# Kernel optimization log

Measured on AMD Instinct MI355X. Metric: run time of the kernel, lower is better.

## Reference

```python
import jax, jax.numpy as jnp
import numpy as np
from jax import lax

# ---- Loihi neuron constants (params['neuron'], params['simulation']) ----
VTH_MANT = 80
THETA = VTH_MANT * (1 << 6)          # 5120, vThMant scaled by 2^6 weight resolution
I_DECAY = 1024                        # current decay (12-bit fixed point)
V_DECAY = 128                         # voltage decay (12-bit fixed point)
WGT_EXP = 0
WGT_SCALE = 1 << (6 + WGT_EXP)        # 64
TS = 1.0

def _loihi_srm_kernel():
    # integer Loihi simulation of the PSP impulse response (slayerLoihi._calculateLoihiPSP)
    u = 1 << (6 + WGT_EXP)
    v = u
    ker = [v]
    while ker[-1] > 0:
        u = (u * (4096 - I_DECAY)) >> 12
        v = ((v * (4096 - V_DECAY)) >> 12) + u
        ker.append(v)
    return np.asarray(ker, np.float32) / (1 << 6)

SRM_KERNEL = _loihi_srm_kernel()      # ~180 taps, ker[0] = 1

def psp(x):
    # causal FIR over time: y[t] = sum_k x[t-k] * ker[k];  x: [B, C, T]
    B, C, T = x.shape
    K = SRM_KERNEL.shape[0]
    w = jnp.asarray(SRM_KERNEL[::-1].copy()).reshape(1, 1, K).astype(x.dtype)
    y = lax.conv_general_dilated(x.reshape(B * C, 1, T), w, (1,), [(K - 1, 0)],
                                 dimension_numbers=('NCH', 'OIH', 'NCH'))
    return y.reshape(B, C, T)

def _decay(x, d):
    # sign-symmetric arithmetic-shift decay, exactly as the Loihi CUDA kernel
    s = jnp.where(x >= 0, 1, -1).astype(jnp.int32)
    return s * ((s * x * (4096 - d)) >> 12)

def spike_loihi(w):
    # quantized integrate-and-fire; w: [B, C, T] float weighted input
    x = jnp.trunc(w * (WGT_SCALE / TS)).astype(jnp.int32)   # C-style int() truncation
    xt = jnp.moveaxis(x, -1, 0)                             # [T, B, C]
    z = jnp.zeros(x.shape[:-1], jnp.int32)
    def step(carry, xi):
        u, v = carry
        un = _decay(u, I_DECAY) + xi
        vn = _decay(v, V_DECAY) + un
        sp = vn >= THETA
        vn = jnp.where(sp, 0, vn)                           # hard reset on spike
        return (un, vn), (sp, vn)
    _, (s, vrec) = lax.scan(step, (z, z), xt)
    spike = jnp.moveaxis(s, 0, -1).astype(w.dtype) / TS
    voltage = jnp.moveaxis(vrec, 0, -1).astype(w.dtype)
    return spike, voltage

def delay_shift(x):
    # delayShift(x, 1): one-tick axonal delay along time
    return jnp.concatenate([jnp.zeros_like(x[..., :1]), x[..., :-1]], axis=-1)

def setup_inputs():
    key = jax.random.key(0)
    k1, k2, k3 = jax.random.split(key, 3)
    B, CIN, HID, COUT, T = 32, 512, 1024, 256, 512
    spike_input = (jax.random.uniform(k1, (B, CIN, 1, 1, T)) < 0.05).astype(jnp.float32)
    W1 = jax.random.normal(k2, (HID, CIN), jnp.float32) * 0.2
    W2 = jax.random.normal(k3, (COUT, HID), jnp.float32) * 0.2
    return {"spike_input": spike_input, "W1": W1, "W2": W2}

def reference(spike_input, W1, W2):
    x = spike_input[:, :, 0, 0, :]                          # [B, Cin, T]
    s1, _ = spike_loihi(psp(jnp.einsum('oi,bit->bot', W1, x)))
    s1 = delay_shift(s1)
    s2, _ = spike_loihi(psp(jnp.einsum('oh,bht->bot', W2, s1)))
    s2 = delay_shift(s2)
    return s2[:, :, None, None, :]                          # [B, Cout, 1, 1, T]
```

## Files before the change

kernel.cpp:

```cpp
#include <hip/hip_runtime.h>


#pragma clang fp contract(off)

constexpr int kT     = 512;
constexpr int kCIN   = 512;
constexpr int kHID   = 1024;
constexpr int kCOUT  = 256;
constexpr int kB     = 32;
constexpr int kTHETA = 5120;
constexpr int kOT1   = 16;
constexpr int kOT2   = 8;
constexpr int kHP1   = 20;
constexpr int kHP2   = 12;
constexpr int kSBP   = 516;
constexpr int kCURP  = 522;
constexpr int kLCAP  = 128;

struct Ker { float v[96]; int n; };
constexpr Ker mk_ker() {
    Ker K{}; int u = 64, v = 64; K.v[0] = 1.0f; int i = 1;
    while (v > 0 && i < 96) {
        u = (u * 3072) >> 12;
        v = ((v * 3968) >> 12) + u;
        K.v[i++] = (float)v / 64.0f;
    }
    K.n = i; return K;
}
constexpr Ker KER = mk_ker();
static_assert(KER.n == 88, "SRM kernel length must be 88");
static_assert(KER.v[87] == 0.0f, "tap 87 must be the exact zero tail tap");
__device__ __constant__ Ker KERC = mk_ker();

__device__ __forceinline__ float2 pkmul(const float2 a, const float b) {
    return make_float2(a.x * b, a.y * b);
}
__device__ __forceinline__ float2 pkadd(const float2 a, const float2 b) {
    return make_float2(a.x + b.x, a.y + b.y);
}

__device__ __forceinline__ int decay_i(int x, int mult) {
    unsigned ax = (x >= 0) ? (unsigned)x : (0u - (unsigned)x);
    unsigned p  = ax * (unsigned)mult;
    int sh = ((int)p) >> 12;
    return (x >= 0) ? sh : (int)(0u - (unsigned)sh);
}

__global__ __launch_bounds__(256) void k0_pack(const float* __restrict__ X,
                                               unsigned* __restrict__ XPW) {
    const int tid = blockIdx.x * 256 + threadIdx.x;
    const int b = tid >> 13, rem = tid & 8191, w = rem >> 9, t = rem & 511;
    const float* xp = X + ((size_t)(b * kCIN + w * 32)) * kT + t;
    unsigned m = 0;
#pragma unroll
    for (int k = 0; k < 32; ++k)
        m |= (xp[(size_t)k * kT] != 0.0f ? 1u : 0u) << k;
    XPW[tid] = m;
}

__global__ __launch_bounds__(256) void k0b_list(const unsigned* __restrict__ XPW,
                                                unsigned short* __restrict__ XL,
                                                unsigned short* __restrict__ XC) {
    const int bt = blockIdx.x * 256 + threadIdx.x;
    const int b = bt >> 9, t = bt & 511;
    const unsigned* xw = XPW + ((size_t)b * 16) * kT + t;
    unsigned short* row = XL + (size_t)bt * kLCAP;
    int cnt = 0;
    for (int w = 0; w < 16; ++w) {
        unsigned m = xw[(size_t)w * kT];
        while (m) {
            const int bi = __ffs(m) - 1; m &= m - 1;
            if (cnt < kLCAP) row[cnt] = (unsigned short)(w * 32 + bi);
            ++cnt;
        }
    }
    XC[bt] = (unsigned short)min(cnt, kLCAP);
}

#define GADD16(II) { const int ii_ = (II); \
    const float4 f0 = *reinterpret_cast<const float4*>(&w0[ii_ * 4]); \
    const float4 f1 = *reinterpret_cast<const float4*>(&w1[ii_ * 4]); \
    const float4 f2 = *reinterpret_cast<const float4*>(&w2[ii_ * 4]); \
    const float4 f3 = *reinterpret_cast<const float4*>(&w3[ii_ * 4]); \
    A0 = pkadd(A0, make_float2(f0.x, f0.y)); A1 = pkadd(A1, make_float2(f0.z, f0.w)); \
    A2 = pkadd(A2, make_float2(f1.x, f1.y)); A3 = pkadd(A3, make_float2(f1.z, f1.w)); \
    A4 = pkadd(A4, make_float2(f2.x, f2.y)); A5 = pkadd(A5, make_float2(f2.z, f2.w)); \
    A6 = pkadd(A6, make_float2(f3.x, f3.y)); A7 = pkadd(A7, make_float2(f3.z, f3.w)); }

#define ACC16(E0,E1,E2,E3,E4,E5,E6,E7, Q0,Q1,Q2,Q3, KV) \
    E0 = pkadd(E0, pkmul(make_float2(Q0.x, Q0.y), (KV))); \
    E1 = pkadd(E1, pkmul(make_float2(Q0.z, Q0.w), (KV))); \
    E2 = pkadd(E2, pkmul(make_float2(Q1.x, Q1.y), (KV))); \
    E3 = pkadd(E3, pkmul(make_float2(Q1.z, Q1.w), (KV))); \
    E4 = pkadd(E4, pkmul(make_float2(Q2.x, Q2.y), (KV))); \
    E5 = pkadd(E5, pkmul(make_float2(Q2.z, Q2.w), (KV))); \
    E6 = pkadd(E6, pkmul(make_float2(Q3.x, Q3.y), (KV))); \
    E7 = pkadd(E7, pkmul(make_float2(Q3.z, Q3.w), (KV)));

__global__ __launch_bounds__(512, 6) void k1_fused(const unsigned short* __restrict__ XL,
                                                   const unsigned short* __restrict__ XC,
                                                   const float* __restrict__ W,
                                                   unsigned short* __restrict__ SPW) {
    __shared__ __align__(16) unsigned char regn[40960];
    __shared__ unsigned char sbuf[kOT1 * kSBP];

    float* w0    = reinterpret_cast<float*>(regn);
    float* w1    = reinterpret_cast<float*>(regn + 8192);
    float* w2    = reinterpret_cast<float*>(regn + 16384);
    float* w3    = reinterpret_cast<float*>(regn + 24576);
    float* heven = reinterpret_cast<float*>(regn);
    float* hodd  = reinterpret_cast<float*>(regn + 20480);
    int*   cur   = reinterpret_cast<int*>(regn);

    const int t     = threadIdx.x;
    const int b     = blockIdx.x >> 6;
    const int oblk  = blockIdx.x & 63;
    const int obase = oblk * kOT1;

    for (int idx = t; idx < kOT1 * kCIN; idx += 512) {
        const int j = idx >> 9, i = idx & 511;
        float* wq = reinterpret_cast<float*>(regn + (j >> 2) * 8192);
        wq[i * 4 + (j & 3)] = W[(size_t)(obase + j) * kCIN + i];
    }
    __syncthreads();

    const int bt = (b << 9) | t;
    const int cnt = XC[bt];
    const uint4* lrow = reinterpret_cast<const uint4*>(XL + (size_t)bt * kLCAP);
    float2 A0 = make_float2(0.f, 0.f), A1 = A0, A2 = A0, A3 = A0,
           A4 = A0, A5 = A0, A6 = A0, A7 = A0;
    for (int k8 = 0; k8 * 8 < cnt; ++k8) {
        const uint4 le = lrow[k8];
        const int base = k8 * 8;
#define GE1(E, V) if (base + (E) < cnt) GADD16((int)(V))
        GE1(0, le.x & 0xffffu) GE1(1, le.x >> 16)
        GE1(2, le.y & 0xffffu) GE1(3, le.y >> 16)
        GE1(4, le.z & 0xffffu) GE1(5, le.z >> 16)
        GE1(6, le.w & 0xffffu) GE1(7, le.w >> 16)
#undef GE1
    }
    __syncthreads();

    {
        float* hr = ((t & 1) ? hodd : heven) + (size_t)(t >> 1) * kHP1;
        *reinterpret_cast<float4*>(hr + 0)  = make_float4(A0.x, A0.y, A1.x, A1.y);
        *reinterpret_cast<float4*>(hr + 4)  = make_float4(A2.x, A2.y, A3.x, A3.y);
        *reinterpret_cast<float4*>(hr + 8)  = make_float4(A4.x, A4.y, A5.x, A5.y);
        *reinterpret_cast<float4*>(hr + 12) = make_float4(A6.x, A6.y, A7.x, A7.y);
    }
    __syncthreads();

    float2 E0, E1, E2, E3, E4, E5, E6, E7, O0, O1, O2, O3, O4, O5, O6, O7;
    E0=E1=E2=E3=E4=E5=E6=E7=O0=O1=O2=O3=O4=O5=O6=O7 = make_float2(0.f, 0.f);
    const int q = t;
    if (t < 256) {
        for (int j = 0; j < 43; ++j) {
            const int m = q - 43 + j;
            const float t87 = KERC.v[87 - 2 * j];
            const float t86 = KERC.v[86 - 2 * j];
            const float t85 = KERC.v[85 - 2 * j];
            if (m >= 0) {
                const float* he = heven + (size_t)m * kHP1;
                const float* ho = hodd  + (size_t)m * kHP1;
                const float4 a0 = *reinterpret_cast<const float4*>(he + 0);
                const float4 a1 = *reinterpret_cast<const float4*>(he + 4);
                const float4 a2 = *reinterpret_cast<const float4*>(he + 8);
                const float4 a3 = *reinterpret_cast<const float4*>(he + 12);
                const float4 b0 = *reinterpret_cast<const float4*>(ho + 0);
                const float4 b1 = *reinterpret_cast<const float4*>(ho + 4);
                const float4 b2 = *reinterpret_cast<const float4*>(ho + 8);
                const float4 b3 = *reinterpret_cast<const float4*>(ho + 12);
                ACC16(E0,E1,E2,E3,E4,E5,E6,E7, a0,a1,a2,a3, t86)
                ACC16(E0,E1,E2,E3,E4,E5,E6,E7, b0,b1,b2,b3, t85)
                ACC16(O0,O1,O2,O3,O4,O5,O6,O7, a0,a1,a2,a3, t87)
                ACC16(O0,O1,O2,O3,O4,O5,O6,O7, b0,b1,b2,b3, t86)
            }
        }
        {
            const float* he = heven + (size_t)q * kHP1;
            const float* ho = hodd  + (size_t)q * kHP1;
            const float4 a0 = *reinterpret_cast<const float4*>(he + 0);
            const float4 a1 = *reinterpret_cast<const float4*>(he + 4);
            const float4 a2 = *reinterpret_cast<const float4*>(he + 8);
            const float4 a3 = *reinterpret_cast<const float4*>(he + 12);
            const float4 b0 = *reinterpret_cast<const float4*>(ho + 0);
            const float4 b1 = *reinterpret_cast<const float4*>(ho + 4);
            const float4 b2 = *reinterpret_cast<const float4*>(ho + 8);
            const float4 b3 = *reinterpret_cast<const float4*>(ho + 12);
            const float v1 = KERC.v[1];
            ACC16(E0,E1,E2,E3,E4,E5,E6,E7, a0,a1,a2,a3, 1.0f)
            ACC16(O0,O1,O2,O3,O4,O5,O6,O7, a0,a1,a2,a3, v1)
            ACC16(O0,O1,O2,O3,O4,O5,O6,O7, b0,b1,b2,b3, 1.0f)
        }
    }
    __syncthreads();

    if (t < 256) {
#define CST1(CH, EV, OV) \
        *reinterpret_cast<int2*>(cur + (CH) * kCURP + 2 * q) = \
            make_int2((int)((EV) * 64.0f), (int)((OV) * 64.0f));
        CST1( 0, E0.x, O0.x) CST1( 1, E0.y, O0.y)
        CST1( 2, E1.x, O1.x) CST1( 3, E1.y, O1.y)
        CST1( 4, E2.x, O2.x) CST1( 5, E2.y, O2.y)
        CST1( 6, E3.x, O3.x) CST1( 7, E3.y, O3.y)
        CST1( 8, E4.x, O4.x) CST1( 9, E4.y, O4.y)
        CST1(10, E5.x, O5.x) CST1(11, E5.y, O5.y)
        CST1(12, E6.x, O6.x) CST1(13, E6.y, O6.y)
        CST1(14, E7.x, O7.x) CST1(15, E7.y, O7.y)
#undef CST1
    }
    __syncthreads();

    if (t < kOT1) {
        const int2* cr2 = reinterpret_cast<const int2*>(cur + t * kCURP);
        int u = 0, v = 0;
        sbuf[t * kSBP + 0] = 0;
        for (int s2 = 0; s2 < 256; ++s2) {
            const int2 c2 = cr2[s2];
            {
                const int un = (int)((unsigned)decay_i(u, 3072) + (unsigned)c2.x);
                int vn = (int)((unsigned)decay_i(v, 3968) + (unsigned)un);
                const int sp_ = (vn >= kTHETA) ? 1 : 0;
                if (sp_) vn = 0;
                u = un; v = vn;
                sbuf[t * kSBP + 2 * s2 + 1] = (unsigned char)sp_;
            }
            {
                const int un = (int)((unsigned)decay_i(u, 3072) + (unsigned)c2.y);
                int vn = (int)((unsigned)decay_i(v, 3968) + (unsigned)un);
                const int sp_ = (vn >= kTHETA) ? 1 : 0;
                if (sp_) vn = 0;
                u = un; v = vn;
                if (2 * s2 + 2 < kT) sbuf[t * kSBP + 2 * s2 + 2] = (unsigned char)sp_;
            }
        }
    }
    __syncthreads();

    {
        unsigned lo = 0, hi = 0;
#pragma unroll
        for (int j = 0; j < 8; ++j) {
            lo |= (unsigned)sbuf[j * kSBP + t] << j;
            hi |= (unsigned)sbuf[(8 + j) * kSBP + t] << j;
        }
        SPW[((((size_t)b * 32 + (oblk >> 1)) * kT) + t) * 2 + (oblk & 1)] =
            (unsigned short)(lo | (hi << 8));
    }
}

#define GW8(MW, BASE) { unsigned m_ = (MW); while (m_) { \
    const int bi_ = __ffs(m_) - 1; m_ &= m_ - 1; const int ii_ = (BASE) + bi_; \
    const float4 lo = *reinterpret_cast<const float4*>(&wlo[ii_ * 4]); \
    const float4 hi = *reinterpret_cast<const float4*>(&whi[ii_ * 4]); \
    A0 = pkadd(A0, make_float2(lo.x, lo.y)); A1 = pkadd(A1, make_float2(lo.z, lo.w)); \
    A2 = pkadd(A2, make_float2(hi.x, hi.y)); A3 = pkadd(A3, make_float2(hi.z, hi.w)); } }

#define ACC8(E0,E1,E2,E3, Q0,Q1, KV) \
    E0 = pkadd(E0, pkmul(make_float2(Q0.x, Q0.y), (KV))); \
    E1 = pkadd(E1, pkmul(make_float2(Q0.z, Q0.w), (KV))); \
    E2 = pkadd(E2, pkmul(make_float2(Q1.x, Q1.y), (KV))); \
    E3 = pkadd(E3, pkmul(make_float2(Q1.z, Q1.w), (KV)));

__global__ __launch_bounds__(512, 8) void k2_fused(const unsigned* __restrict__ SPW,
                                                   const float* __restrict__ W,
                                                   float* __restrict__ O) {
    __shared__ __align__(16) unsigned char regn[32768];
    __shared__ unsigned char sbuf[kOT2 * kSBP];

    float* wlo   = reinterpret_cast<float*>(regn);
    float* whi   = reinterpret_cast<float*>(regn + 16384);
    float* heven = reinterpret_cast<float*>(regn);
    float* hodd  = reinterpret_cast<float*>(regn + 12288);
    int*   cur   = reinterpret_cast<int*>(regn);

    const int t     = threadIdx.x;
    const int b     = blockIdx.x >> 5;
    const int obase = (blockIdx.x & 31) * kOT2;

    for (int idx = t; idx < kOT2 * kHID; idx += 512) {
        const int j = idx >> 10, i = idx & 1023;
        const float w = W[(size_t)(obase + j) * kHID + i];
        if (j < 4) wlo[i * 4 + j] = w; else whi[i * 4 + (j - 4)] = w;
    }
    __syncthreads();

    const unsigned* sp = SPW + ((size_t)b * 32) * kT + t;
    float2 A0 = make_float2(0.f, 0.f), A1 = A0, A2 = A0, A3 = A0;
#pragma unroll 4
    for (int g = 0; g < 32; ++g) {
        const unsigned m = sp[(size_t)g * kT];
        GW8(m, g * 32)
    }
    __syncthreads();

    {
        float* hr = ((t & 1) ? hodd : heven) + (size_t)(t >> 1) * kHP2;
        *reinterpret_cast<float4*>(hr + 0) = make_float4(A0.x, A0.y, A1.x, A1.y);
        *reinterpret_cast<float4*>(hr + 4) = make_float4(A2.x, A2.y, A3.x, A3.y);
    }
    __syncthreads();

    float2 E0, E1, E2, E3, O0, O1, O2, O3;
    E0=E1=E2=E3=O0=O1=O2=O3 = make_float2(0.f, 0.f);
    const int q = t;
    if (t < 256) {
        for (int j = 0; j < 43; ++j) {
            const int m = q - 43 + j;
            const float t87 = KERC.v[87 - 2 * j];
            const float t86 = KERC.v[86 - 2 * j];
            const float t85 = KERC.v[85 - 2 * j];
            if (m >= 0) {
                const float* he = heven + (size_t)m * kHP2;
                const float* ho = hodd  + (size_t)m * kHP2;
                const float4 a0 = *reinterpret_cast<const float4*>(he + 0);
                const float4 a1 = *reinterpret_cast<const float4*>(he + 4);
                const float4 b0 = *reinterpret_cast<const float4*>(ho + 0);
                const float4 b1 = *reinterpret_cast<const float4*>(ho + 4);
                ACC8(E0,E1,E2,E3, a0,a1, t86)
                ACC8(E0,E1,E2,E3, b0,b1, t85)
                ACC8(O0,O1,O2,O3, a0,a1, t87)
                ACC8(O0,O1,O2,O3, b0,b1, t86)
            }
        }
        {
            const float* he = heven + (size_t)q * kHP2;
            const float* ho = hodd  + (size_t)q * kHP2;
            const float4 a0 = *reinterpret_cast<const float4*>(he + 0);
            const float4 a1 = *reinterpret_cast<const float4*>(he + 4);
            const float4 b0 = *reinterpret_cast<const float4*>(ho + 0);
            const float4 b1 = *reinterpret_cast<const float4*>(ho + 4);
            const float v1 = KERC.v[1];
            ACC8(E0,E1,E2,E3, a0,a1, 1.0f)
            ACC8(O0,O1,O2,O3, a0,a1, v1)
            ACC8(O0,O1,O2,O3, b0,b1, 1.0f)
        }
    }
    __syncthreads();

    if (t < 256) {
#define CST2(CH, EV, OV) \
        *reinterpret_cast<int2*>(cur + (CH) * kCURP + 2 * q) = \
            make_int2((int)((EV) * 64.0f), (int)((OV) * 64.0f));
        CST2(0, E0.x, O0.x) CST2(1, E0.y, O0.y)
        CST2(2, E1.x, O1.x) CST2(3, E1.y, O1.y)
        CST2(4, E2.x, O2.x) CST2(5, E2.y, O2.y)
        CST2(6, E3.x, O3.x) CST2(7, E3.y, O3.y)
#undef CST2
    }
    __syncthreads();

    if (t < kOT2) {
        const int2* cr2 = reinterpret_cast<const int2*>(cur + t * kCURP);
        int u = 0, v = 0;
        sbuf[t * kSBP + 0] = 0;
        for (int s2 = 0; s2 < 256; ++s2) {
            const int2 c2 = cr2[s2];
            {
                const int un = (int)((unsigned)decay_i(u, 3072) + (unsigned)c2.x);
                int vn = (int)((unsigned)decay_i(v, 3968) + (unsigned)un);
                const int sp2 = (vn >= kTHETA) ? 1 : 0;
                if (sp2) vn = 0;
                u = un; v = vn;
                sbuf[t * kSBP + 2 * s2 + 1] = (unsigned char)sp2;
            }
            {
                const int un = (int)((unsigned)decay_i(u, 3072) + (unsigned)c2.y);
                int vn = (int)((unsigned)decay_i(v, 3968) + (unsigned)un);
                const int sp2 = (vn >= kTHETA) ? 1 : 0;
                if (sp2) vn = 0;
                u = un; v = vn;
                if (2 * s2 + 2 < kT) sbuf[t * kSBP + 2 * s2 + 2] = (unsigned char)sp2;
            }
        }
    }
    __syncthreads();

    for (int idx = t; idx < kOT2 * kT; idx += 512) {
        const int j = idx >> 9, tt = idx & 511;
        O[((size_t)(b * kCOUT + obase + j)) * kT + tt] = (float)sbuf[j * kSBP + tt];
    }
}

__global__ void k_mark(float* __restrict__ out0, float v) {
    if (threadIdx.x == 0 && blockIdx.x == 0) out0[0] = v;
}

extern "C" void kernel_launch(void* const* d_in, const int* in_sizes, int n_in,
                              void* d_out, int out_size, void* d_ws, size_t ws_size,
                              hipStream_t stream) {
    const float* X  = (const float*)d_in[0];
    const float* W1 = (const float*)d_in[1];
    const float* W2 = (const float*)d_in[2];
    float* OUT = (float*)d_out;

    const size_t xpw_bytes = (size_t)kB * 16 * kT * 4;
    const size_t spw_bytes = (size_t)kB * 32 * kT * 4;
    const size_t xl_bytes  = (size_t)kB * kT * kLCAP * 2;
    const size_t xc_bytes  = (size_t)kB * kT * 2;
    const size_t need = xpw_bytes + spw_bytes + xl_bytes + xc_bytes;

    if (n_in != 3 || in_sizes[0] != kB * kCIN * kT || in_sizes[1] != kHID * kCIN ||
        in_sizes[2] != kCOUT * kHID || out_size != kB * kCOUT * kT) {
        hipLaunchKernelGGL(k_mark, dim3(1), dim3(64), 0, stream, OUT, 7000001.0f);
        return;
    }
    if (ws_size < need || d_ws == nullptr) {
        const float v = (float)(8000000u + (unsigned)((ws_size >> 10) % 900000));
        hipLaunchKernelGGL(k_mark, dim3(1), dim3(64), 0, stream, OUT, v);
        return;
    }

    char* ws = (char*)d_ws;
    unsigned*       xpw = (unsigned*)ws;
    unsigned short* spw = (unsigned short*)(ws + xpw_bytes);
    unsigned short* xl  = (unsigned short*)(ws + xpw_bytes + spw_bytes);
    unsigned short* xc  = (unsigned short*)(ws + xpw_bytes + spw_bytes + xl_bytes);

    hipLaunchKernelGGL(k0_pack, dim3(kB * 16 * kT / 256), dim3(256), 0, stream,
                       X, xpw);
    hipLaunchKernelGGL(k0b_list, dim3(kB * kT / 256), dim3(256), 0, stream,
                       xpw, xl, xc);
    hipLaunchKernelGGL(k1_fused, dim3(kB * (kHID / kOT1)), dim3(512), 0, stream,
                       xl, xc, W1, spw);
    hipLaunchKernelGGL(k2_fused, dim3(kB * (kCOUT / kOT2)), dim3(512), 0, stream,
                       (const unsigned*)spw, W2, OUT);
}
```

Baseline: 390.5 us.

## Move part of weight tiles from LDS to pre-packed global reads; split PSP across all threads

Result: slower. 442.6 us (+13.3%).

```diff
diff --git a/kernel.cpp b/kernel.cpp
--- a/kernel.cpp
+++ b/kernel.cpp
@@ -77,29 +77,40 @@
     XC[bt] = (unsigned short)min(cnt, kLCAP);
 }
 
+__global__ __launch_bounds__(256) void k0c_w1p(const float* __restrict__ W1,
+                                               float* __restrict__ W1P) {
+    const int tid = blockIdx.x * 256 + threadIdx.x;
+    const int c = tid & 3, i = (tid >> 2) & 511, oblk = tid >> 11;
+    W1P[tid] = W1[(size_t)(oblk * 16 + 12 + c) * kCIN + i];
+}
+
+__global__ __launch_bounds__(256) void k0d_w2p(const float* __restrict__ W2,
+                                               float* __restrict__ W2P) {
+    const int tid = blockIdx.x * 256 + threadIdx.x;
+    const int c = tid & 3, i = (tid >> 2) & 1023, o2 = tid >> 12;
+    W2P[tid] = W2[(size_t)(o2 * 8 + 4 + c) * kHID + i];
+}
+
 #define GADD16(II) { const int ii_ = (II); \
     const float4 f0 = *reinterpret_cast<const float4*>(&w0[ii_ * 4]); \
     const float4 f1 = *reinterpret_cast<const float4*>(&w1[ii_ * 4]); \
     const float4 f2 = *reinterpret_cast<const float4*>(&w2[ii_ * 4]); \
-    const float4 f3 = *reinterpret_cast<const float4*>(&w3[ii_ * 4]); \
+    const float4 f3 = w1p4[ii_];   \
     A0 = pkadd(A0, make_float2(f0.x, f0.y)); A1 = pkadd(A1, make_float2(f0.z, f0.w)); \
     A2 = pkadd(A2, make_float2(f1.x, f1.y)); A3 = pkadd(A3, make_float2(f1.z, f1.w)); \
     A4 = pkadd(A4, make_float2(f2.x, f2.y)); A5 = pkadd(A5, make_float2(f2.z, f2.w)); \
     A6 = pkadd(A6, make_float2(f3.x, f3.y)); A7 = pkadd(A7, make_float2(f3.z, f3.w)); }
 
-#define ACC16(E0,E1,E2,E3,E4,E5,E6,E7, Q0,Q1,Q2,Q3, KV) \
+#define ACC8(E0,E1,E2,E3, Q0,Q1, KV) \
     E0 = pkadd(E0, pkmul(make_float2(Q0.x, Q0.y), (KV))); \
     E1 = pkadd(E1, pkmul(make_float2(Q0.z, Q0.w), (KV))); \
     E2 = pkadd(E2, pkmul(make_float2(Q1.x, Q1.y), (KV))); \
-    E3 = pkadd(E3, pkmul(make_float2(Q1.z, Q1.w), (KV))); \
-    E4 = pkadd(E4, pkmul(make_float2(Q2.x, Q2.y), (KV))); \
-    E5 = pkadd(E5, pkmul(make_float2(Q2.z, Q2.w), (KV))); \
-    E6 = pkadd(E6, pkmul(make_float2(Q3.x, Q3.y), (KV))); \
-    E7 = pkadd(E7, pkmul(make_float2(Q3.z, Q3.w), (KV)));
+    E3 = pkadd(E3, pkmul(make_float2(Q1.z, Q1.w), (KV)));
 
 __global__ __launch_bounds__(512, 6) void k1_fused(const unsigned short* __restrict__ XL,
                                                    const unsigned short* __restrict__ XC,
                                                    const float* __restrict__ W,
+                                                   const float* __restrict__ W1P,
                                                    unsigned short* __restrict__ SPW) {
     __shared__ __align__(16) unsigned char regn[40960];
     __shared__ unsigned char sbuf[kOT1 * kSBP];
@@ -107,7 +118,6 @@
     float* w0    = reinterpret_cast<float*>(regn);
     float* w1    = reinterpret_cast<float*>(regn + 8192);
     float* w2    = reinterpret_cast<float*>(regn + 16384);
-    float* w3    = reinterpret_cast<float*>(regn + 24576);
     float* heven = reinterpret_cast<float*>(regn);
     float* hodd  = reinterpret_cast<float*>(regn + 20480);
     int*   cur   = reinterpret_cast<int*>(regn);
@@ -117,7 +127,9 @@
     const int oblk  = blockIdx.x & 63;
     const int obase = oblk * kOT1;
 
-    for (int idx = t; idx < kOT1 * kCIN; idx += 512) {
+    const float4* w1p4 = reinterpret_cast<const float4*>(W1P + (size_t)oblk * kCIN * 4);
+
+    for (int idx = t; idx < 12 * kCIN; idx += 512) {
         const int j = idx >> 9, i = idx & 511;
         float* wq = reinterpret_cast<float*>(regn + (j >> 2) * 8192);
         wq[i * 4 + (j & 3)] = W[(size_t)(obase + j) * kCIN + i];
@@ -150,63 +162,49 @@
     }
     __syncthreads();
 
-    float2 E0, E1, E2, E3, E4, E5, E6, E7, O0, O1, O2, O3, O4, O5, O6, O7;
-    E0=E1=E2=E3=E4=E5=E6=E7=O0=O1=O2=O3=O4=O5=O6=O7 = make_float2(0.f, 0.f);
-    const int q = t;
-    if (t < 256) {
-        for (int j = 0; j < 43; ++j) {
-            const int m = q - 43 + j;
-            const float t87 = KERC.v[87 - 2 * j];
-            const float t86 = KERC.v[86 - 2 * j];
-            const float t85 = KERC.v[85 - 2 * j];
-            if (m >= 0) {
-                const float* he = heven + (size_t)m * kHP1;
-                const float* ho = hodd  + (size_t)m * kHP1;
-                const float4 a0 = *reinterpret_cast<const float4*>(he + 0);
-                const float4 a1 = *reinterpret_cast<const float4*>(he + 4);
-                const float4 a2 = *reinterpret_cast<const float4*>(he + 8);
-                const float4 a3 = *reinterpret_cast<const float4*>(he + 12);
-                const float4 b0 = *reinterpret_cast<const float4*>(ho + 0);
-                const float4 b1 = *reinterpret_cast<const float4*>(ho + 4);
-                const float4 b2 = *reinterpret_cast<const float4*>(ho + 8);
-                const float4 b3 = *reinterpret_cast<const float4*>(ho + 12);
-                ACC16(E0,E1,E2,E3,E4,E5,E6,E7, a0,a1,a2,a3, t86)
-                ACC16(E0,E1,E2,E3,E4,E5,E6,E7, b0,b1,b2,b3, t85)
-                ACC16(O0,O1,O2,O3,O4,O5,O6,O7, a0,a1,a2,a3, t87)
-                ACC16(O0,O1,O2,O3,O4,O5,O6,O7, b0,b1,b2,b3, t86)
-            }
-        }
-        {
-            const float* he = heven + (size_t)q * kHP1;
-            const float* ho = hodd  + (size_t)q * kHP1;
+    const int p = t & 255, half = t >> 8, hoff = half * 8;
+    float2 E0, E1, E2, E3, O0, O1, O2, O3;
+    E0=E1=E2=E3=O0=O1=O2=O3 = make_float2(0.f, 0.f);
+    for (int j = 0; j < 43; ++j) {
+        const int m = p - 43 + j;
+        const float t87 = KERC.v[87 - 2 * j];
+        const float t86 = KERC.v[86 - 2 * j];
+        const float t85 = KERC.v[85 - 2 * j];
+        if (m >= 0) {
+            const float* he = heven + (size_t)m * kHP1 + hoff;
+            const float* ho = hodd  + (size_t)m * kHP1 + hoff;
             const float4 a0 = *reinterpret_cast<const float4*>(he + 0);
             const float4 a1 = *reinterpret_cast<const float4*>(he + 4);
-            const float4 a2 = *reinterpret_cast<const float4*>(he + 8);
-            const float4 a3 = *reinterpret_cast<const float4*>(he + 12);
             const float4 b0 = *reinterpret_cast<const float4*>(ho + 0);
             const float4 b1 = *reinterpret_cast<const float4*>(ho + 4);
-            const float4 b2 = *reinterpret_cast<const float4*>(ho + 8);
-            const float4 b3 = *reinterpret_cast<const float4*>(ho + 12);
-            const float v1 = KERC.v[1];
-            ACC16(E0,E1,E2,E3,E4,E5,E6,E7, a0,a1,a2,a3, 1.0f)
-            ACC16(O0,O1,O2,O3,O4,O5,O6,O7, a0,a1,a2,a3, v1)
-            ACC16(O0,O1,O2,O3,O4,O5,O6,O7, b0,b1,b2,b3, 1.0f)
-        }
-    }
-    __syncthreads();
-
-    if (t < 256) {
+            ACC8(E0,E1,E2,E3, a0,a1, t86)
+            ACC8(E0,E1,E2,E3, b0,b1, t85)
+            ACC8(O0,O1,O2,O3, a0,a1, t87)
+            ACC8(O0,O1,O2,O3, b0,b1, t86)
+        }
+    }
+    {
+        const float* he = heven + (size_t)p * kHP1 + hoff;
+        const float* ho = hodd  + (size_t)p * kHP1 + hoff;
+        const float4 a0 = *reinterpret_cast<const float4*>(he + 0);
+        const float4 a1 = *reinterpret_cast<const float4*>(he + 4);
+        const float4 b0 = *reinterpret_cast<const float4*>(ho + 0);
+        const float4 b1 = *reinterpret_cast<const float4*>(ho + 4);
+        const float v1 = KERC.v[1];
+        ACC8(E0,E1,E2,E3, a0,a1, 1.0f)
+        ACC8(O0,O1,O2,O3, a0,a1, v1)
+        ACC8(O0,O1,O2,O3, b0,b1, 1.0f)
+    }
+    __syncthreads();
+
+    {
 #define CST1(CH, EV, OV) \
-        *reinterpret_cast<int2*>(cur + (CH) * kCURP + 2 * q) = \
+        *reinterpret_cast<int2*>(cur + (CH) * kCURP + 2 * p) = \
             make_int2((int)((EV) * 64.0f), (int)((OV) * 64.0f));
-        CST1( 0, E0.x, O0.x) CST1( 1, E0.y, O0.y)
-        CST1( 2, E1.x, O1.x) CST1( 3, E1.y, O1.y)
-        CST1( 4, E2.x, O2.x) CST1( 5, E2.y, O2.y)
-        CST1( 6, E3.x, O3.x) CST1( 7, E3.y, O3.y)
-        CST1( 8, E4.x, O4.x) CST1( 9, E4.y, O4.y)
-        CST1(10, E5.x, O5.x) CST1(11, E5.y, O5.y)
-        CST1(12, E6.x, O6.x) CST1(13, E6.y, O6.y)
-        CST1(14, E7.x, O7.x) CST1(15, E7.y, O7.y)
+        CST1(hoff + 0, E0.x, O0.x) CST1(hoff + 1, E0.y, O0.y)
+        CST1(hoff + 2, E1.x, O1.x) CST1(hoff + 3, E1.y, O1.y)
+        CST1(hoff + 4, E2.x, O2.x) CST1(hoff + 5, E2.y, O2.y)
+        CST1(hoff + 6, E3.x, O3.x) CST1(hoff + 7, E3.y, O3.y)
 #undef CST1
     }
     __syncthreads();
@@ -252,36 +250,32 @@
 #define GW8(MW, BASE) { unsigned m_ = (MW); while (m_) { \
     const int bi_ = __ffs(m_) - 1; m_ &= m_ - 1; const int ii_ = (BASE) + bi_; \
     const float4 lo = *reinterpret_cast<const float4*>(&wlo[ii_ * 4]); \
-    const float4 hi = *reinterpret_cast<const float4*>(&whi[ii_ * 4]); \
+    const float4 hi = w2p4[ii_];   \
     A0 = pkadd(A0, make_float2(lo.x, lo.y)); A1 = pkadd(A1, make_float2(lo.z, lo.w)); \
     A2 = pkadd(A2, make_float2(hi.x, hi.y)); A3 = pkadd(A3, make_float2(hi.z, hi.w)); } }
 
-#define ACC8(E0,E1,E2,E3, Q0,Q1, KV) \
-    E0 = pkadd(E0, pkmul(make_float2(Q0.x, Q0.y), (KV))); \
-    E1 = pkadd(E1, pkmul(make_float2(Q0.z, Q0.w), (KV))); \
-    E2 = pkadd(E2, pkmul(make_float2(Q1.x, Q1.y), (KV))); \
-    E3 = pkadd(E3, pkmul(make_float2(Q1.z, Q1.w), (KV)));
-
 __global__ __launch_bounds__(512, 8) void k2_fused(const unsigned* __restrict__ SPW,
                                                    const float* __restrict__ W,
+                                                   const float* __restrict__ W2P,
                                                    float* __restrict__ O) {
-    __shared__ __align__(16) unsigned char regn[32768];
+    __shared__ __align__(16) unsigned char regn[24576];
     __shared__ unsigned char sbuf[kOT2 * kSBP];
 
     float* wlo   = reinterpret_cast<float*>(regn);
-    float* whi   = reinterpret_cast<float*>(regn + 16384);
     float* heven = reinterpret_cast<float*>(regn);
     float* hodd  = reinterpret_cast<float*>(regn + 12288);
     int*   cur   = reinterpret_cast<int*>(regn);
 
     const int t     = threadIdx.x;
     const int b     = blockIdx.x >> 5;
-    const int obase = (blockIdx.x & 31) * kOT2;
-
-    for (int idx = t; idx < kOT2 * kHID; idx += 512) {
+    const int o2    = blockIdx.x & 31;
+    const int obase = o2 * kOT2;
+
+    const float4* w2p4 = reinterpret_cast<const float4*>(W2P + (size_t)o2 * kHID * 4);
+
+    for (int idx = t; idx < 4 * kHID; idx += 512) {
         const int j = idx >> 10, i = idx & 1023;
-        const float w = W[(size_t)(obase + j) * kHID + i];
-        if (j < 4) wlo[i * 4 + j] = w; else whi[i * 4 + (j - 4)] = w;
+        wlo[i * 4 + j] = W[(size_t)(obase + j) * kHID + i];
     }
     __syncthreads();
 
@@ -398,7 +392,10 @@
     const size_t spw_bytes = (size_t)kB * 32 * kT * 4;
     const size_t xl_bytes  = (size_t)kB * kT * kLCAP * 2;
     const size_t xc_bytes  = (size_t)kB * kT * 2;
-    const size_t need = xpw_bytes + spw_bytes + xl_bytes + xc_bytes;
+    const size_t w1p_bytes = (size_t)64 * kCIN * 4 * 4;
+    const size_t w2p_bytes = (size_t)32 * kHID * 4 * 4;
+    const size_t need = xpw_bytes + spw_bytes + xl_bytes + xc_bytes +
+                        w1p_bytes + w2p_bytes;
 
     if (n_in != 3 || in_sizes[0] != kB * kCIN * kT || in_sizes[1] != kHID * kCIN ||
         in_sizes[2] != kCOUT * kHID || out_size != kB * kCOUT * kT) {
@@ -416,13 +413,19 @@
     unsigned short* spw = (unsigned short*)(ws + xpw_bytes);
     unsigned short* xl  = (unsigned short*)(ws + xpw_bytes + spw_bytes);
     unsigned short* xc  = (unsigned short*)(ws + xpw_bytes + spw_bytes + xl_bytes);
+    float*          w1p = (float*)(ws + xpw_bytes + spw_bytes + xl_bytes + xc_bytes);
+    float*          w2p = (float*)(ws + xpw_bytes + spw_bytes + xl_bytes + xc_bytes + w1p_bytes);
 
     hipLaunchKernelGGL(k0_pack, dim3(kB * 16 * kT / 256), dim3(256), 0, stream,
                        X, xpw);
     hipLaunchKernelGGL(k0b_list, dim3(kB * kT / 256), dim3(256), 0, stream,
                        xpw, xl, xc);
+    hipLaunchKernelGGL(k0c_w1p, dim3(64 * kCIN * 4 / 256), dim3(256), 0, stream,
+                       W1, w1p);
+    hipLaunchKernelGGL(k0d_w2p, dim3(32 * kHID * 4 / 256), dim3(256), 0, stream,
+                       W2, w2p);
     hipLaunchKernelGGL(k1_fused, dim3(kB * (kHID / kOT1)), dim3(512), 0, stream,
-                       xl, xc, W1, spw);
+                       xl, xc, W1, w1p, spw);
     hipLaunchKernelGGL(k2_fused, dim3(kB * (kCOUT / kOT2)), dim3(512), 0, stream,
-                       (const unsigned*)spw, W2, OUT);
-}
+                       (const unsigned*)spw, W2, w2p, OUT);
+}
```

## Use all 512 threads for layer-1 PSP with 4-phase polyphase split

Applied to the files above, without the earlier changes.

New measurement: 381.0 us (median of 3 runs). 1.02x faster.

```diff
diff --git a/kernel.cpp b/kernel.cpp
--- a/kernel.cpp
+++ b/kernel.cpp
@@ -14,7 +14,8 @@
 constexpr int kHP1   = 20;
 constexpr int kHP2   = 12;
 constexpr int kSBP   = 516;
-constexpr int kCURP  = 522;
+constexpr int kCURP1 = 524;
+constexpr int kCURP2 = 522;
 constexpr int kLCAP  = 128;
 
 struct Ker { float v[96]; int n; };
@@ -87,15 +88,9 @@
     A4 = pkadd(A4, make_float2(f2.x, f2.y)); A5 = pkadd(A5, make_float2(f2.z, f2.w)); \
     A6 = pkadd(A6, make_float2(f3.x, f3.y)); A7 = pkadd(A7, make_float2(f3.z, f3.w)); }
 
-#define ACC16(E0,E1,E2,E3,E4,E5,E6,E7, Q0,Q1,Q2,Q3, KV) \
-    E0 = pkadd(E0, pkmul(make_float2(Q0.x, Q0.y), (KV))); \
-    E1 = pkadd(E1, pkmul(make_float2(Q0.z, Q0.w), (KV))); \
-    E2 = pkadd(E2, pkmul(make_float2(Q1.x, Q1.y), (KV))); \
-    E3 = pkadd(E3, pkmul(make_float2(Q1.z, Q1.w), (KV))); \
-    E4 = pkadd(E4, pkmul(make_float2(Q2.x, Q2.y), (KV))); \
-    E5 = pkadd(E5, pkmul(make_float2(Q2.z, Q2.w), (KV))); \
-    E6 = pkadd(E6, pkmul(make_float2(Q3.x, Q3.y), (KV))); \
-    E7 = pkadd(E7, pkmul(make_float2(Q3.z, Q3.w), (KV)));
+#define ACCROW(CA, CB, R, KV) \
+    CA = pkadd(CA, pkmul(make_float2((R).x, (R).y), (KV))); \
+    CB = pkadd(CB, pkmul(make_float2((R).z, (R).w), (KV)));
 
 __global__ __launch_bounds__(512, 6) void k1_fused(const unsigned short* __restrict__ XL,
                                                    const unsigned short* __restrict__ XC,
@@ -104,13 +99,11 @@
     __shared__ __align__(16) unsigned char regn[40960];
     __shared__ unsigned char sbuf[kOT1 * kSBP];
 
-    float* w0    = reinterpret_cast<float*>(regn);
-    float* w1    = reinterpret_cast<float*>(regn + 8192);
-    float* w2    = reinterpret_cast<float*>(regn + 16384);
-    float* w3    = reinterpret_cast<float*>(regn + 24576);
-    float* heven = reinterpret_cast<float*>(regn);
-    float* hodd  = reinterpret_cast<float*>(regn + 20480);
-    int*   cur   = reinterpret_cast<int*>(regn);
+    float* w0 = reinterpret_cast<float*>(regn);
+    float* w1 = reinterpret_cast<float*>(regn + 8192);
+    float* w2 = reinterpret_cast<float*>(regn + 16384);
+    float* w3 = reinterpret_cast<float*>(regn + 24576);
+    int*   cur = reinterpret_cast<int*>(regn);
 
     const int t     = threadIdx.x;
     const int b     = blockIdx.x >> 6;
@@ -142,7 +135,8 @@
     __syncthreads();
 
     {
-        float* hr = ((t & 1) ? hodd : heven) + (size_t)(t >> 1) * kHP1;
+        float* hr = reinterpret_cast<float*>(regn + (t & 3) * 10240)
+                    + (size_t)(t >> 2) * kHP1;
         *reinterpret_cast<float4*>(hr + 0)  = make_float4(A0.x, A0.y, A1.x, A1.y);
         *reinterpret_cast<float4*>(hr + 4)  = make_float4(A2.x, A2.y, A3.x, A3.y);
         *reinterpret_cast<float4*>(hr + 8)  = make_float4(A4.x, A4.y, A5.x, A5.y);
@@ -150,69 +144,59 @@
     }
     __syncthreads();
 
-    float2 E0, E1, E2, E3, E4, E5, E6, E7, O0, O1, O2, O3, O4, O5, O6, O7;
-    E0=E1=E2=E3=E4=E5=E6=E7=O0=O1=O2=O3=O4=O5=O6=O7 = make_float2(0.f, 0.f);
-    const int q = t;
-    if (t < 256) {
-        for (int j = 0; j < 43; ++j) {
-            const int m = q - 43 + j;
-            const float t87 = KERC.v[87 - 2 * j];
-            const float t86 = KERC.v[86 - 2 * j];
-            const float t85 = KERC.v[85 - 2 * j];
-            if (m >= 0) {
-                const float* he = heven + (size_t)m * kHP1;
-                const float* ho = hodd  + (size_t)m * kHP1;
-                const float4 a0 = *reinterpret_cast<const float4*>(he + 0);
-                const float4 a1 = *reinterpret_cast<const float4*>(he + 4);
-                const float4 a2 = *reinterpret_cast<const float4*>(he + 8);
-                const float4 a3 = *reinterpret_cast<const float4*>(he + 12);
-                const float4 b0 = *reinterpret_cast<const float4*>(ho + 0);
-                const float4 b1 = *reinterpret_cast<const float4*>(ho + 4);
-                const float4 b2 = *reinterpret_cast<const float4*>(ho + 8);
-                const float4 b3 = *reinterpret_cast<const float4*>(ho + 12);
-                ACC16(E0,E1,E2,E3,E4,E5,E6,E7, a0,a1,a2,a3, t86)
-                ACC16(E0,E1,E2,E3,E4,E5,E6,E7, b0,b1,b2,b3, t85)
-                ACC16(O0,O1,O2,O3,O4,O5,O6,O7, a0,a1,a2,a3, t87)
-                ACC16(O0,O1,O2,O3,O4,O5,O6,O7, b0,b1,b2,b3, t86)
-            }
-        }
-        {
-            const float* he = heven + (size_t)q * kHP1;
-            const float* ho = hodd  + (size_t)q * kHP1;
-            const float4 a0 = *reinterpret_cast<const float4*>(he + 0);
-            const float4 a1 = *reinterpret_cast<const float4*>(he + 4);
-            const float4 a2 = *reinterpret_cast<const float4*>(he + 8);
-            const float4 a3 = *reinterpret_cast<const float4*>(he + 12);
-            const float4 b0 = *reinterpret_cast<const float4*>(ho + 0);
-            const float4 b1 = *reinterpret_cast<const float4*>(ho + 4);
-            const float4 b2 = *reinterpret_cast<const float4*>(ho + 8);
-            const float4 b3 = *reinterpret_cast<const float4*>(ho + 12);
-            const float v1 = KERC.v[1];
-            ACC16(E0,E1,E2,E3,E4,E5,E6,E7, a0,a1,a2,a3, 1.0f)
-            ACC16(O0,O1,O2,O3,O4,O5,O6,O7, a0,a1,a2,a3, v1)
-            ACC16(O0,O1,O2,O3,O4,O5,O6,O7, b0,b1,b2,b3, 1.0f)
-        }
-    }
-    __syncthreads();
-
-    if (t < 256) {
-#define CST1(CH, EV, OV) \
-        *reinterpret_cast<int2*>(cur + (CH) * kCURP + 2 * q) = \
-            make_int2((int)((EV) * 64.0f), (int)((OV) * 64.0f));
-        CST1( 0, E0.x, O0.x) CST1( 1, E0.y, O0.y)
-        CST1( 2, E1.x, O1.x) CST1( 3, E1.y, O1.y)
-        CST1( 4, E2.x, O2.x) CST1( 5, E2.y, O2.y)
-        CST1( 6, E3.x, O3.x) CST1( 7, E3.y, O3.y)
-        CST1( 8, E4.x, O4.x) CST1( 9, E4.y, O4.y)
-        CST1(10, E5.x, O5.x) CST1(11, E5.y, O5.y)
-        CST1(12, E6.x, O6.x) CST1(13, E6.y, O6.y)
-        CST1(14, E7.x, O7.x) CST1(15, E7.y, O7.y)
-#undef CST1
+    const int q = t & 127, qt = t >> 7, coff = qt * 4;
+    float2 C0a, C0b, C1a, C1b, C2a, C2b, C3a, C3b;
+    C0a=C0b=C1a=C1b=C2a=C2b=C3a=C3b = make_float2(0.f, 0.f);
+    const float* h0 = reinterpret_cast<const float*>(regn)        + coff;
+    const float* h1 = reinterpret_cast<const float*>(regn + 10240) + coff;
+    const float* h2 = reinterpret_cast<const float*>(regn + 20480) + coff;
+    const float* h3 = reinterpret_cast<const float*>(regn + 30720) + coff;
+    for (int s = 22; s >= 0; --s) {
+        const int m = q - s;
+        if (m < 0) continue;
+        float tp[7];
+#pragma unroll
+        for (int z = 0; z < 7; ++z) {
+            const int tau = 4 * s - 3 + z;
+            tp[z] = ((unsigned)tau < 88u) ? KERC.v[tau] : 0.0f;
+        }
+        const float4 r0 = *reinterpret_cast<const float4*>(h0 + (size_t)m * kHP1);
+        const float4 r1 = *reinterpret_cast<const float4*>(h1 + (size_t)m * kHP1);
+        const float4 r2 = *reinterpret_cast<const float4*>(h2 + (size_t)m * kHP1);
+        const float4 r3 = *reinterpret_cast<const float4*>(h3 + (size_t)m * kHP1);
+        ACCROW(C0a, C0b, r0, tp[3]) ACCROW(C0a, C0b, r1, tp[2])
+        ACCROW(C0a, C0b, r2, tp[1]) ACCROW(C0a, C0b, r3, tp[0])
+        ACCROW(C1a, C1b, r0, tp[4]) ACCROW(C1a, C1b, r1, tp[3])
+        ACCROW(C1a, C1b, r2, tp[2]) ACCROW(C1a, C1b, r3, tp[1])
+        ACCROW(C2a, C2b, r0, tp[5]) ACCROW(C2a, C2b, r1, tp[4])
+        ACCROW(C2a, C2b, r2, tp[3]) ACCROW(C2a, C2b, r3, tp[2])
+        ACCROW(C3a, C3b, r0, tp[6]) ACCROW(C3a, C3b, r1, tp[5])
+        ACCROW(C3a, C3b, r2, tp[4]) ACCROW(C3a, C3b, r3, tp[3])
+    }
+    __syncthreads();
+
+    {
+        int* c0 = cur + (coff + 0) * kCURP1 + 4 * q;
+        int* c1 = cur + (coff + 1) * kCURP1 + 4 * q;
+        int* c2 = cur + (coff + 2) * kCURP1 + 4 * q;
+        int* c3 = cur + (coff + 3) * kCURP1 + 4 * q;
+        *reinterpret_cast<int4*>(c0) = make_int4(
+            (int)(C0a.x * 64.0f), (int)(C1a.x * 64.0f),
+            (int)(C2a.x * 64.0f), (int)(C3a.x * 64.0f));
+        *reinterpret_cast<int4*>(c1) = make_int4(
+            (int)(C0a.y * 64.0f), (int)(C1a.y * 64.0f),
+            (int)(C2a.y * 64.0f), (int)(C3a.y * 64.0f));
+        *reinterpret_cast<int4*>(c2) = make_int4(
+            (int)(C0b.x * 64.0f), (int)(C1b.x * 64.0f),
+            (int)(C2b.x * 64.0f), (int)(C3b.x * 64.0f));
+        *reinterpret_cast<int4*>(c3) = make_int4(
+            (int)(C0b.y * 64.0f), (int)(C1b.y * 64.0f),
+            (int)(C2b.y * 64.0f), (int)(C3b.y * 64.0f));
     }
     __syncthreads();
 
     if (t < kOT1) {
-        const int2* cr2 = reinterpret_cast<const int2*>(cur + t * kCURP);
+        const int2* cr2 = reinterpret_cast<const int2*>(cur + t * kCURP1);
         int u = 0, v = 0;
         sbuf[t * kSBP + 0] = 0;
         for (int s2 = 0; s2 < 256; ++s2) {
@@ -340,7 +324,7 @@
 
     if (t < 256) {
 #define CST2(CH, EV, OV) \
-        *reinterpret_cast<int2*>(cur + (CH) * kCURP + 2 * q) = \
+        *reinterpret_cast<int2*>(cur + (CH) * kCURP2 + 2 * q) = \
             make_int2((int)((EV) * 64.0f), (int)((OV) * 64.0f));
         CST2(0, E0.x, O0.x) CST2(1, E0.y, O0.y)
         CST2(2, E1.x, O1.x) CST2(3, E1.y, O1.y)
@@ -351,7 +335,7 @@
     __syncthreads();
 
     if (t < kOT2) {
-        const int2* cr2 = reinterpret_cast<const int2*>(cur + t * kCURP);
+        const int2* cr2 = reinterpret_cast<const int2*>(cur + t * kCURP2);
         int u = 0, v = 0;
         sbuf[t * kSBP + 0] = 0;
         for (int s2 = 0; s2 < 256; ++s2) {
```
